# Kernel tuning notes

Hardware: AMD Instinct MI355X
Metric: run time of the kernel (lower is better)

Reference implementation:

```python
import jax, jax.numpy as jnp
import numpy as np

IN_F = 256
OUT_F = 64
LRELU_SLOPE = 0.2


def setup_inputs() -> dict:
    key = jax.random.key(0)
    k1, k2, k3 = jax.random.split(key, 3)
    B, N = 4, 4096
    h = jax.random.normal(k1, (B, N, IN_F), dtype=jnp.float32)
    # xavier_uniform with gain=1.414
    def xavier(k, shape, gain=1.414):
        fan_in, fan_out = shape[0], shape[1]
        bound = gain * np.sqrt(6.0 / (fan_in + fan_out))
        return jax.random.uniform(k, shape, jnp.float32, -bound, bound)
    W = xavier(k2, (IN_F, OUT_F))
    a = xavier(k3, (2 * OUT_F, 1))
    return {"h": h, "W": W, "a": a}


def reference(h, W, a):
    # Wh: (B, N, F_out)
    Wh = jnp.matmul(h, W)
    # Algebraic split of a = [a1; a2]: score(i,j) = Wh_i @ a1 + Wh_j @ a2
    a1 = a[:OUT_F, 0]   # (F,)
    a2 = a[OUT_F:, 0]   # (F,)
    e1 = Wh @ a1        # (B, N)
    e2 = Wh @ a2        # (B, N)
    e = e1[:, :, None] + e2[:, None, :]   # (B, N, N)
    return jnp.where(e > 0, e, LRELU_SLOPE * e)
```

## Files before the change

kernel.cpp:

```cpp
#include <hip/hip_runtime.h>
#include <hip/hip_bf16.h>


#define B_DIM 4
#define N_DIM 4096
#define IN_F 256
#define OUT_F 64
#define SLOPE 0.2f

__global__ void gat_compute_v(const float* __restrict__ W, const float* __restrict__ a,
                              float* __restrict__ v ) {
    int k = threadIdx.x;
    float s1 = 0.f, s2 = 0.f;
    const float* wr = W + k * OUT_F;
    #pragma unroll 8
    for (int j = 0; j < OUT_F; ++j) {
        float w = wr[j];
        s1 += w * a[j];
        s2 += w * a[OUT_F + j];
    }
    v[k] = s1;
    v[IN_F + k] = s2;
}

__global__ void gat_row_dots(const float* __restrict__ h, const float* __restrict__ v,
                             float* __restrict__ e1, float* __restrict__ e2) {
    int gid  = blockIdx.x * blockDim.x + threadIdx.x;
    int row  = gid >> 6;
    int lane = threadIdx.x & 63;
    if (row >= B_DIM * N_DIM) return;

    const float4 hv = reinterpret_cast<const float4*>(h + (size_t)row * IN_F)[lane];
    const float4 v1 = reinterpret_cast<const float4*>(v)[lane];
    const float4 v2 = reinterpret_cast<const float4*>(v + IN_F)[lane];

    float d1 = hv.x * v1.x + hv.y * v1.y + hv.z * v1.z + hv.w * v1.w;
    float d2 = hv.x * v2.x + hv.y * v2.y + hv.z * v2.z + hv.w * v2.w;

    #pragma unroll
    for (int m = 32; m >= 1; m >>= 1) {
        d1 += __shfl_xor(d1, m);
        d2 += __shfl_xor(d2, m);
    }
    if (lane == 0) {
        e1[row] = d1;
        e2[row] = d2;
    }
}

__global__ void gat_epilogue(const float* __restrict__ e1, const float* __restrict__ e2,
                             float* __restrict__ out) {
    const int total4 = B_DIM * N_DIM * (N_DIM / 4);
    const int stride = gridDim.x * blockDim.x;
    const float4* e2v = reinterpret_cast<const float4*>(e2);
    float4* outv = reinterpret_cast<float4*>(out);

    for (int idx = blockIdx.x * blockDim.x + threadIdx.x; idx < total4; idx += stride) {
        int row = idx >> 10;
        int c4  = idx & 1023;
        int b   = row >> 12;
        float s = e1[row];
        float4 t = e2v[b * (N_DIM / 4) + c4];
        float4 o;
        float ex = s + t.x; o.x = fmaxf(ex, SLOPE * ex);
        float ey = s + t.y; o.y = fmaxf(ey, SLOPE * ey);
        float ez = s + t.z; o.z = fmaxf(ez, SLOPE * ez);
        float ew = s + t.w; o.w = fmaxf(ew, SLOPE * ew);
        outv[idx] = o;
    }
}

extern "C" void kernel_launch(void* const* d_in, const int* in_sizes, int n_in,
                              void* d_out, int out_size, void* d_ws, size_t ws_size,
                              hipStream_t stream) {
    const float* h = (const float*)d_in[0];
    const float* W = (const float*)d_in[1];
    const float* a = (const float*)d_in[2];

    float* ws = (float*)d_ws;
    float* v  = ws;
    float* e1 = ws + 512;
    float* e2 = ws + 512 + 16384;

    gat_compute_v<<<1, 256, 0, stream>>>(W, a, v);

    const int rows = B_DIM * N_DIM;
    gat_row_dots<<<rows * 64 / 256, 256, 0, stream>>>(h, v, e1, e2);

    gat_epilogue<<<2048, 256, 0, stream>>>(e1, e2, (float*)d_out);
}
```

Baseline: 59.25 us.

## Fuse v computation into row-dot kernel and use per-row nontemporal epilogue

Folds the W·a projection into the row-dot kernel, where each block recomputes v into shared memory, which removes one kernel launch. Each block now covers 64 rows with 16 rows per wave. The epilogue becomes one block per output row, using a single broadcast e1 load and nontemporal stores for the 256MB output. In exchange, every one of the 256 blocks redundantly reads W (64KB), and the row-dot kernel runs fewer, longer-lived waves.

```diff
diff --git a/kernel.cpp b/kernel.cpp
--- a/kernel.cpp
+++ b/kernel.cpp
@@ -8,65 +8,70 @@
 #define OUT_F 64
 #define SLOPE 0.2f
 
-__global__ void gat_compute_v(const float* __restrict__ W, const float* __restrict__ a,
-                              float* __restrict__ v ) {
-    int k = threadIdx.x;
-    float s1 = 0.f, s2 = 0.f;
-    const float* wr = W + k * OUT_F;
-    #pragma unroll 8
-    for (int j = 0; j < OUT_F; ++j) {
-        float w = wr[j];
-        s1 += w * a[j];
-        s2 += w * a[OUT_F + j];
+typedef float f32x4 __attribute__((ext_vector_type(4)));
+
+__global__ void gat_dots(const float* __restrict__ h, const float* __restrict__ W,
+                         const float* __restrict__ a,
+                         float* __restrict__ e1, float* __restrict__ e2) {
+    __shared__ float v1s[IN_F];
+    __shared__ float v2s[IN_F];
+    const int t = threadIdx.x;
+
+    {
+        float s1 = 0.f, s2 = 0.f;
+        const float* wr = W + t * OUT_F;
+        #pragma unroll 8
+        for (int j = 0; j < OUT_F; ++j) {
+            float w = wr[j];
+            s1 += w * a[j];
+            s2 += w * a[OUT_F + j];
+        }
+        v1s[t] = s1;
+        v2s[t] = s2;
     }
-    v[k] = s1;
-    v[IN_F + k] = s2;
-}
+    __syncthreads();
 
-__global__ void gat_row_dots(const float* __restrict__ h, const float* __restrict__ v,
-                             float* __restrict__ e1, float* __restrict__ e2) {
-    int gid  = blockIdx.x * blockDim.x + threadIdx.x;
-    int row  = gid >> 6;
-    int lane = threadIdx.x & 63;
-    if (row >= B_DIM * N_DIM) return;
+    const int lane = t & 63;
+    const int wid  = t >> 6;
+    const f32x4 v1 = reinterpret_cast<const f32x4*>(v1s)[lane];
+    const f32x4 v2 = reinterpret_cast<const f32x4*>(v2s)[lane];
+    const int base = blockIdx.x * 64 + wid * 16;
 
-    const float4 hv = reinterpret_cast<const float4*>(h + (size_t)row * IN_F)[lane];
-    const float4 v1 = reinterpret_cast<const float4*>(v)[lane];
-    const float4 v2 = reinterpret_cast<const float4*>(v + IN_F)[lane];
-
-    float d1 = hv.x * v1.x + hv.y * v1.y + hv.z * v1.z + hv.w * v1.w;
-    float d2 = hv.x * v2.x + hv.y * v2.y + hv.z * v2.z + hv.w * v2.w;
-
-    #pragma unroll
-    for (int m = 32; m >= 1; m >>= 1) {
-        d1 += __shfl_xor(d1, m);
-        d2 += __shfl_xor(d2, m);
-    }
-    if (lane == 0) {
-        e1[row] = d1;
-        e2[row] = d2;
+    for (int r = 0; r < 16; ++r) {
+        const int row = base + r;
+        const f32x4 hv = reinterpret_cast<const f32x4*>(h + (size_t)row * IN_F)[lane];
+        float d1 = hv.x * v1.x + hv.y * v1.y + hv.z * v1.z + hv.w * v1.w;
+        float d2 = hv.x * v2.x + hv.y * v2.y + hv.z * v2.z + hv.w * v2.w;
+        #pragma unroll
+        for (int m = 32; m >= 1; m >>= 1) {
+            d1 += __shfl_xor(d1, m);
+            d2 += __shfl_xor(d2, m);
+        }
+        if (lane == 0) {
+            e1[row] = d1;
+            e2[row] = d2;
+        }
     }
 }
 
 __global__ void gat_epilogue(const float* __restrict__ e1, const float* __restrict__ e2,
                              float* __restrict__ out) {
-    const int total4 = B_DIM * N_DIM * (N_DIM / 4);
-    const int stride = gridDim.x * blockDim.x;
-    const float4* e2v = reinterpret_cast<const float4*>(e2);
-    float4* outv = reinterpret_cast<float4*>(out);
+    const int row = blockIdx.x;
+    const int b   = row >> 12;
+    const float s = e1[row];
+    const f32x4* e2v = reinterpret_cast<const f32x4*>(e2 + b * N_DIM);
+    f32x4* outv = reinterpret_cast<f32x4*>(out + (size_t)row * N_DIM);
 
-    for (int idx = blockIdx.x * blockDim.x + threadIdx.x; idx < total4; idx += stride) {
-        int row = idx >> 10;
-        int c4  = idx & 1023;
-        int b   = row >> 12;
-        float s = e1[row];
-        float4 t = e2v[b * (N_DIM / 4) + c4];
-        float4 o;
+    #pragma unroll
+    for (int k = 0; k < 4; ++k) {
+        const int c = threadIdx.x + k * 256;
+        const f32x4 t = e2v[c];
+        f32x4 o;
         float ex = s + t.x; o.x = fmaxf(ex, SLOPE * ex);
         float ey = s + t.y; o.y = fmaxf(ey, SLOPE * ey);
         float ez = s + t.z; o.z = fmaxf(ez, SLOPE * ez);
         float ew = s + t.w; o.w = fmaxf(ew, SLOPE * ew);
-        outv[idx] = o;
+        __builtin_nontemporal_store(o, &outv[c]);
     }
 }
 
@@ -78,14 +83,9 @@
     const float* a = (const float*)d_in[2];
 
     float* ws = (float*)d_ws;
-    float* v  = ws;
-    float* e1 = ws + 512;
-    float* e2 = ws + 512 + 16384;
+    float* e1 = ws;
+    float* e2 = ws + 16384;
 
-    gat_compute_v<<<1, 256, 0, stream>>>(W, a, v);
-
-    const int rows = B_DIM * N_DIM;
-    gat_row_dots<<<rows * 64 / 256, 256, 0, stream>>>(h, v, e1, e2);
-
-    gat_epilogue<<<2048, 256, 0, stream>>>(e1, e2, (float*)d_out);
+    gat_dots<<<256, 256, 0, stream>>>(h, W, a, e1, e2);
+    gat_epilogue<<<B_DIM * N_DIM, 256, 0, stream>>>(e1, e2, (float*)d_out);
 }
```

New measurement: 62.26 us. 5.1% more time.
